# Optimization experiments

Hardware: AMD Instinct MI355X
Metric: run time of the kernel (lower is better)

Reference implementation:

```python
import jax, jax.numpy as jnp
import numpy as np
import math

SIZE = 64
NLAND = 8
N_ITER = 6


def setup_inputs() -> dict:
    key = jax.random.key(0)
    k1, k2, k3 = jax.random.split(key, 3)
    B, T, C = 4, 4096, 1024
    return {
        "q": jax.random.normal(k1, (B, T, C), dtype=jnp.float32),
        "k": jax.random.normal(k2, (B, T, C), dtype=jnp.float32),
        "v": jax.random.normal(k3, (B, T, C), dtype=jnp.float32),
    }


def _iterative_pinv(mat, n_iter=N_ITER):
    # Newton-Schulz iteration for pseudo-inverse of [..., m, m] kernel.
    m = mat.shape[-1]
    I = jnp.eye(m, dtype=mat.dtype)
    K = mat
    # NOTE: torch.max over the whole tensor (global scalar), faithful to source.
    V = (1.0 / jnp.max(jnp.sum(K, axis=-2))) * jnp.swapaxes(K, -1, -2)
    for _ in range(n_iter):
        KV = jnp.matmul(K, V)
        V = jnp.matmul(0.25 * V, 13.0 * I - jnp.matmul(KV, 15.0 * I - jnp.matmul(KV, 7.0 * I - KV)))
    return V


def reference(q, k, v):
    B, T, C = q.shape
    H = C // SIZE
    scale = 1.0 / math.sqrt(SIZE)
    # Faithful reshape (not transpose) as in the source module.
    qh = q.reshape(B, H, T, SIZE)
    kh = k.reshape(B, H, T, SIZE)
    vh = v.reshape(B, H, T, SIZE)
    # T % NLAND == 0 branch: landmark = segment mean over T//NLAND tokens.
    q_l = qh.reshape(B, H, NLAND, T // NLAND, SIZE).mean(axis=-2)  # [B,H,m,d]
    k_l = kh.reshape(B, H, NLAND, T // NLAND, SIZE).mean(axis=-2)
    kernel_1 = jax.nn.softmax(jnp.einsum('bhtd,bhmd->bhtm', qh, k_l) * scale, axis=-1)  # [B,H,T,m]
    kernel_2 = jax.nn.softmax(jnp.einsum('bhmd,bhnd->bhmn', q_l, k_l) * scale, axis=-1)  # [B,H,m,m]
    kernel_3 = jax.nn.softmax(jnp.einsum('bhmd,bhtd->bhmt', q_l, kh) * scale, axis=-1)  # [B,H,m,T]
    pinv = _iterative_pinv(kernel_2)  # [B,H,m,m]
    k3v = jnp.matmul(kernel_3, vh)    # [B,H,m,d]
    out = jnp.matmul(jnp.matmul(kernel_1, pinv), k3v)  # [B,H,T,d]
    return out.reshape(B, T, C)
```

## Files before the change

### kernel.cpp

```cpp
#include <hip/hip_runtime.h>
#include <math.h>

#define T_TOK 4096
#define DD 64
#define NHEADS 64
#define SEG 512
#define SCALE 0.125f

#define QL_OFF   0
#define KL_OFF   32768
#define K2_OFF   65536
#define CS_OFF   69632
#define PD_OFF   70144
#define W2_OFF   102912
#define KP_OFF   135680
#define PA_OFF   135680
#define P_OFF    659968

#define WAVE_BAR() __builtin_amdgcn_wave_barrier()

#define ROR_ADD(x, imm)                                                        \
  {                                                                            \
    int t_ = __builtin_amdgcn_update_dpp(0, __float_as_int(x), 0x120 | (imm),  \
                                         0xF, 0xF, false);                     \
    x += __int_as_float(t_);                                                   \
  }

__global__ __launch_bounds__(256) void qsum_kernel(
    const float* __restrict__ q, float* __restrict__ ws) {
  int tid = threadIdx.x;
  const float4* q4 = (const float4*)q + (size_t)blockIdx.x * 8192;
  float4 b[2][8];
#pragma unroll
  for (int i = 0; i < 8; ++i) b[0][i] = q4[i * 256 + tid];
  float4 a = make_float4(0.f, 0.f, 0.f, 0.f);
#pragma unroll
  for (int j = 0; j < 4; ++j) {
    if (j < 3) {
#pragma unroll
      for (int i = 0; i < 8; ++i)
        b[(j + 1) & 1][i] = q4[(j + 1) * 2048 + i * 256 + tid];
    }
#pragma unroll
    for (int i = 0; i < 8; ++i) {
      float4 x = b[j & 1][i];
      a.x += x.x; a.y += x.y; a.z += x.z; a.w += x.w;
    }
  }
  __shared__ float4 red[16][17];
  red[tid >> 4][tid & 15] = a;
  __syncthreads();
  if (tid < 16) {
    float4 s = make_float4(0.f, 0.f, 0.f, 0.f);
#pragma unroll
    for (int g = 0; g < 16; ++g) {
      float4 r = red[g][tid];
      s.x += r.x; s.y += r.y; s.z += r.z; s.w += r.w;
    }
    const float inv = 1.f / (float)SEG;
    s.x *= inv; s.y *= inv; s.z *= inv; s.w *= inv;
    ((float4*)(ws + QL_OFF))[blockIdx.x * 16 + tid] = s;
  }
}

__global__ __launch_bounds__(256, 4) void ppass_kernel(
    const float* __restrict__ k, float* __restrict__ ws) {
  int tid = threadIdx.x;
  int w = tid >> 6, lane = tid & 63;
  int gw = blockIdx.x * 4 + w;
  int hb = gw >> 6;
  int d16 = lane & 15, t4 = lane >> 4;

  float4 ql[8];
#pragma unroll
  for (int j = 0; j < 8; ++j)
    ql[j] = ((const float4*)(ws + QL_OFF))[hb * 128 + j * 16 + d16];

  size_t base4 = (size_t)gw * 1024;
  const float4* k4 = (const float4*)k + base4;
  float4* pP = (float4*)(ws + P_OFF) + (size_t)gw * 128;

  float den[8];
#pragma unroll
  for (int j = 0; j < 8; ++j) den[j] = 0.f;
  float4 ks = make_float4(0.f, 0.f, 0.f, 0.f);

#pragma unroll 2
  for (int it = 0; it < 16; ++it) {
    float4 kk = k4[it * 64 + lane];
    ks.x += kk.x; ks.y += kk.y; ks.z += kk.z; ks.w += kk.w;
    float dp[8];
#pragma unroll
    for (int j = 0; j < 8; ++j)
      dp[j] = kk.x * ql[j].x + kk.y * ql[j].y + kk.z * ql[j].z +
              kk.w * ql[j].w;
#pragma unroll
    for (int j = 0; j < 8; ++j) { ROR_ADD(dp[j], 8) }
#pragma unroll
    for (int j = 0; j < 8; ++j) { ROR_ADD(dp[j], 4) }
#pragma unroll
    for (int j = 0; j < 8; ++j) { ROR_ADD(dp[j], 2) }
#pragma unroll
    for (int j = 0; j < 8; ++j) { ROR_ADD(dp[j], 1) }
    float p[8];
#pragma unroll
    for (int j = 0; j < 8; ++j) {
      p[j] = __expf(dp[j] * SCALE);
      den[j] += p[j];
    }
    float4 lo = make_float4(p[0], p[1], p[2], p[3]);
    float4 hi = make_float4(p[4], p[5], p[6], p[7]);
    int tok2 = (it * 4 + t4) * 2;
    if (d16 == 0) pP[tok2] = lo;
    if (d16 == 1) pP[tok2 + 1] = hi;
  }

  ks.x += __shfl_xor(ks.x, 16, 64); ks.y += __shfl_xor(ks.y, 16, 64);
  ks.z += __shfl_xor(ks.z, 16, 64); ks.w += __shfl_xor(ks.w, 16, 64);
  ks.x += __shfl_xor(ks.x, 32, 64); ks.y += __shfl_xor(ks.y, 32, 64);
  ks.z += __shfl_xor(ks.z, 32, 64); ks.w += __shfl_xor(ks.w, 32, 64);
  if (lane < 16)
    ((float4*)(ws + KP_OFF))[gw * 16 + lane] = ks;
#pragma unroll
  for (int j = 0; j < 8; ++j) {
    den[j] += __shfl_xor(den[j], 16, 64);
    den[j] += __shfl_xor(den[j], 32, 64);
  }
  if (lane == 0) {
    *(float4*)&ws[PD_OFF + (size_t)gw * 8] =
        make_float4(den[0], den[1], den[2], den[3]);
    *(float4*)&ws[PD_OFF + (size_t)gw * 8 + 4] =
        make_float4(den[4], den[5], den[6], den[7]);
  }
}

__global__ __launch_bounds__(512) void prepk_kernel(float* __restrict__ ws) {
  int hb = blockIdx.x, tid = threadIdx.x;
  __shared__ float qls[8][68];
  __shared__ float kls[8][68];
  __shared__ float ee[8][9];
  int m = tid >> 6, d = tid & 63;
  float s = 0.f;
#pragma unroll
  for (int j = 0; j < 8; ++j)
    s += ws[KP_OFF + (size_t)(hb * 64 + m * 8 + j) * 64 + d];
  s *= (1.f / (float)SEG);
  kls[m][d] = s;
  ws[KL_OFF + hb * 512 + tid] = s;
  qls[m][d] = ws[QL_OFF + hb * 512 + tid];
  __syncthreads();
  if (tid < 64) {
    int i = tid >> 3, j = tid & 7;
    float dot = 0.f;
#pragma unroll
    for (int dd = 0; dd < 64; ++dd) dot += qls[i][dd] * kls[j][dd];
    ee[i][j] = __expf(dot * SCALE);
  }
  __syncthreads();
  if (tid < 64) {
    int i = tid >> 3, j = tid & 7;
    float ssum = 0.f;
#pragma unroll
    for (int jj = 0; jj < 8; ++jj) ssum += ee[i][jj];
    ws[K2_OFF + hb * 64 + tid] = ee[i][j] / ssum;
  }
  if (tid < 8) {
    float cs = 0.f;
    for (int ii = 0; ii < 8; ++ii) {
      float ssum = 0.f;
#pragma unroll
      for (int jj = 0; jj < 8; ++jj) ssum += ee[ii][jj];
      cs += ee[ii][tid] / ssum;
    }
    ws[CS_OFF + hb * 8 + tid] = cs;
  }
}

__global__ __launch_bounds__(256, 4) void vpass_kernel(
    const float* __restrict__ v, float* __restrict__ ws) {
  int tid = threadIdx.x;
  int w = tid >> 6, lane = tid & 63;
  int chunk = blockIdx.x;
  int gw = chunk * 4 + w;
  int t4 = lane >> 4;

  size_t base4 = (size_t)gw * 1024;
  const float4* v4 = (const float4*)v + base4;
  const float4* pP = (const float4*)(ws + P_OFF) + (size_t)gw * 128;

  float4 acc[8];
#pragma unroll
  for (int j = 0; j < 8; ++j) acc[j] = make_float4(0.f, 0.f, 0.f, 0.f);

#pragma unroll 2
  for (int it = 0; it < 16; ++it) {
    float4 vv = v4[it * 64 + lane];
    int tok2 = (it * 4 + t4) * 2;
    float4 plo = pP[tok2];
    float4 phi = pP[tok2 + 1];
    acc[0].x += plo.x*vv.x; acc[0].y += plo.x*vv.y; acc[0].z += plo.x*vv.z; acc[0].w += plo.x*vv.w;
    acc[1].x += plo.y*vv.x; acc[1].y += plo.y*vv.y; acc[1].z += plo.y*vv.z; acc[1].w += plo.y*vv.w;
    acc[2].x += plo.z*vv.x; acc[2].y += plo.z*vv.y; acc[2].z += plo.z*vv.z; acc[2].w += plo.z*vv.w;
    acc[3].x += plo.w*vv.x; acc[3].y += plo.w*vv.y; acc[3].z += plo.w*vv.z; acc[3].w += plo.w*vv.w;
    acc[4].x += phi.x*vv.x; acc[4].y += phi.x*vv.y; acc[4].z += phi.x*vv.z; acc[4].w += phi.x*vv.w;
    acc[5].x += phi.y*vv.x; acc[5].y += phi.y*vv.y; acc[5].z += phi.y*vv.z; acc[5].w += phi.y*vv.w;
    acc[6].x += phi.z*vv.x; acc[6].y += phi.z*vv.y; acc[6].z += phi.z*vv.z; acc[6].w += phi.z*vv.w;
    acc[7].x += phi.w*vv.x; acc[7].y += phi.w*vv.y; acc[7].z += phi.w*vv.z; acc[7].w += phi.w*vv.w;
  }

#pragma unroll
  for (int j = 0; j < 8; ++j) {
    acc[j].x += __shfl_xor(acc[j].x, 16, 64);
    acc[j].y += __shfl_xor(acc[j].y, 16, 64);
    acc[j].z += __shfl_xor(acc[j].z, 16, 64);
    acc[j].w += __shfl_xor(acc[j].w, 16, 64);
    acc[j].x += __shfl_xor(acc[j].x, 32, 64);
    acc[j].y += __shfl_xor(acc[j].y, 32, 64);
    acc[j].z += __shfl_xor(acc[j].z, 32, 64);
    acc[j].w += __shfl_xor(acc[j].w, 32, 64);
  }
  __shared__ float4 accred[4][8][17];
  if (lane < 16) {
#pragma unroll
    for (int j = 0; j < 8; ++j) accred[w][j][lane] = acc[j];
  }
  __syncthreads();
  if (tid < 128) {
    int m = tid >> 4, i = tid & 15;
    float4 a = accred[0][m][i], b = accred[1][m][i];
    float4 c = accred[2][m][i], d2 = accred[3][m][i];
    float4 s = make_float4(a.x + b.x + c.x + d2.x, a.y + b.y + c.y + d2.y,
                           a.z + b.z + c.z + d2.z, a.w + b.w + c.w + d2.w);
    ((float4*)(ws + PA_OFF))[((size_t)chunk * 8 + m) * 16 + i] = s;
  }
}

__global__ __launch_bounds__(512) void pinvw2_kernel(float* __restrict__ ws) {
  int hb = blockIdx.x, tid = threadIdx.x;
  __shared__ float k3vs[8][68];
  __shared__ float K[8][9], V[8][9], X[8][9], Y[8][9];
  __shared__ float smax;
  int m = tid >> 6, d = tid & 63;
  float s = 0.f, den = 0.f;
  for (int c = 0; c < 16; ++c)
    s += ws[PA_OFF + (((size_t)hb * 16 + c) * 8 + m) * 64 + d];
  for (int c = 0; c < 64; ++c)
    den += ws[PD_OFF + ((size_t)hb * 64 + c) * 8 + m];
  k3vs[m][d] = s / den;
  if (tid < 64) {
    float mx = 0.f;
    for (int t = 0; t < 8; ++t) mx = fmaxf(mx, ws[CS_OFF + t * 64 + tid]);
    for (int off = 32; off; off >>= 1) mx = fmaxf(mx, __shfl_xor(mx, off, 64));
    if (tid == 0) smax = mx;
  }
  int i = (tid >> 3) & 7, j = tid & 7;
  if (tid < 64) K[i][j] = ws[K2_OFF + hb * 64 + tid];
  __syncthreads();
  if (tid < 64) V[i][j] = K[j][i] * (1.f / smax);
  __syncthreads();
  for (int it = 0; it < 6; ++it) {
    float x = 0.f;
    if (tid < 64) {
      for (int kk = 0; kk < 8; ++kk) x += K[i][kk] * V[kk][j];
      X[i][j] = x;
    }
    __syncthreads();
    float bm = 0.f;
    if (tid < 64) {
      for (int kk = 0; kk < 8; ++kk) bm += X[i][kk] * X[kk][j];
      bm = 7.f * x - bm;
      Y[i][j] = bm;
    }
    __syncthreads();
    float dm = 0.f;
    if (tid < 64) {
      for (int kk = 0; kk < 8; ++kk) dm += X[i][kk] * Y[kk][j];
      dm = 15.f * x - dm;
    }
    __syncthreads();
    if (tid < 64) Y[i][j] = dm;
    __syncthreads();
    float vd = 0.f;
    if (tid < 64) {
      for (int kk = 0; kk < 8; ++kk) vd += V[i][kk] * Y[kk][j];
      vd = 0.25f * (13.f * V[i][j] - vd);
    }
    __syncthreads();
    if (tid < 64) V[i][j] = vd;
    __syncthreads();
  }
  float o = 0.f;
#pragma unroll
  for (int jj = 0; jj < 8; ++jj) o += V[m][jj] * k3vs[jj][d];
  ws[W2_OFF + hb * 512 + tid] = o;
}

__global__ __launch_bounds__(256) void out_kernel(
    const float* __restrict__ q, float* __restrict__ out,
    const float* __restrict__ ws) {
  int tid = threadIdx.x;
  int w = tid >> 6, lane = tid & 63;
  int gw = blockIdx.x * 4 + w;
  int hb = gw >> 6;
  __shared__ float qt_all[4][16][68];
  __shared__ float pl_all[4][16][9];
  __shared__ float w2_all[4][8][68];
  float (*qt)[68] = qt_all[w];
  float (*pl)[9]  = pl_all[w];
  float (*w2)[68] = w2_all[w];

  int m = lane & 7;
  float4 klrow[16];
#pragma unroll
  for (int d4 = 0; d4 < 16; ++d4)
    klrow[d4] = ((const float4*)(ws + KL_OFF))[hb * 128 + m * 16 + d4];
#pragma unroll
  for (int i = 0; i < 2; ++i) {
    int f4 = i * 64 + lane;
    float4 y = ((const float4*)(ws + W2_OFF))[hb * 128 + f4];
    *(float4*)&w2[f4 >> 4][(f4 & 15) * 4] = y;
  }

  size_t base4 = (size_t)gw * 1024;
  const float4* q4 = (const float4*)q + base4;
  float4* o4 = (float4*)out + base4;
  float4 buf[2][4];
#pragma unroll
  for (int i = 0; i < 4; ++i) buf[0][i] = q4[i * 64 + lane];

#pragma unroll
  for (int tile = 0; tile < 4; ++tile) {
    int cur = tile & 1;
    if (tile < 3) {
#pragma unroll
      for (int i = 0; i < 4; ++i)
        buf[cur ^ 1][i] = q4[(tile + 1) * 256 + i * 64 + lane];
    }
#pragma unroll
    for (int i = 0; i < 4; ++i) {
      int f4 = i * 64 + lane;
      *(float4*)&qt[f4 >> 4][(f4 & 15) * 4] = buf[cur][i];
    }
    WAVE_BAR();
#pragma unroll
    for (int rep = 0; rep < 2; ++rep) {
      int t = rep * 8 + (lane >> 3);
      const float4* qr = (const float4*)&qt[t][0];
      float dot = 0.f;
#pragma unroll
      for (int d4 = 0; d4 < 16; ++d4) {
        float4 a = qr[d4];
        dot += a.x * klrow[d4].x + a.y * klrow[d4].y +
               a.z * klrow[d4].z + a.w * klrow[d4].w;
      }
      pl[t][m] = __expf(dot * SCALE);
    }
    WAVE_BAR();
#pragma unroll
    for (int i = 0; i < 4; ++i) {
      int t = i * 4 + (lane >> 4);
      int qd = lane & 15;
      float p0 = pl[t][0], p1 = pl[t][1], p2 = pl[t][2], p3 = pl[t][3];
      float p4 = pl[t][4], p5 = pl[t][5], p6 = pl[t][6], p7 = pl[t][7];
      float inv = 1.f / (p0 + p1 + p2 + p3 + p4 + p5 + p6 + p7);
      float4 acc = make_float4(0.f, 0.f, 0.f, 0.f);
      float pm[8] = {p0, p1, p2, p3, p4, p5, p6, p7};
#pragma unroll
      for (int m2 = 0; m2 < 8; ++m2) {
        float wgt = pm[m2] * inv;
        float4 wv = *(const float4*)&w2[m2][qd * 4];
        acc.x += wgt * wv.x; acc.y += wgt * wv.y;
        acc.z += wgt * wv.z; acc.w += wgt * wv.w;
      }
      o4[tile * 256 + i * 64 + lane] = acc;
    }
    WAVE_BAR();
  }
}

extern "C" void kernel_launch(void* const* d_in, const int* in_sizes, int n_in,
                              void* d_out, int out_size, void* d_ws, size_t ws_size,
                              hipStream_t stream) {
  const float* q = (const float*)d_in[0];
  const float* k = (const float*)d_in[1];
  const float* v = (const float*)d_in[2];
  float* out = (float*)d_out;
  float* ws = (float*)d_ws;

  qsum_kernel<<<512, 256, 0, stream>>>(q, ws);
  ppass_kernel<<<1024, 256, 0, stream>>>(k, ws);
  prepk_kernel<<<NHEADS, 512, 0, stream>>>(ws);
  vpass_kernel<<<1024, 256, 0, stream>>>(v, ws);
  pinvw2_kernel<<<NHEADS, 512, 0, stream>>>(ws);
  out_kernel<<<1024, 256, 0, stream>>>(q, out, ws);
}
```

Before: 93.79 us.

## Fuse K softmax-weight pass and V accumulation into a single kvpass kernel

Merges the k pass, which computed kernel_3 exp weights and stored them to workspace, with the v pass, which reread those weights to accumulate kernel_3·V. Each wave now keeps the weights in registers and accumulates against V directly. This removes the intermediate P buffer round trip and one kernel launch. Per-wave partials are written out unreduced, and pinvw2 now reduces over 64 wave partials instead of 16 block partials. The trade-off is higher register pressure and more partial traffic in the final reduction.

```diff
diff --git a/kernel.cpp b/kernel.cpp
--- a/kernel.cpp
+++ b/kernel.cpp
@@ -11,11 +11,10 @@
 #define KL_OFF   32768
 #define K2_OFF   65536
 #define CS_OFF   69632
-#define PD_OFF   70144
-#define W2_OFF   102912
-#define KP_OFF   135680
-#define PA_OFF   135680
-#define P_OFF    659968
+#define KP_OFF   70144
+#define PA_OFF   332288
+#define PD_OFF   2429440
+#define W2_OFF   2462208
 
 #define WAVE_BAR() __builtin_amdgcn_wave_barrier()
 
@@ -63,13 +62,35 @@
   }
 }
 
-__global__ __launch_bounds__(256, 4) void ppass_kernel(
-    const float* __restrict__ k, float* __restrict__ ws) {
+#define KV_PROC(KK, VV)                                                        \
+  {                                                                            \
+    ks.x += KK.x; ks.y += KK.y; ks.z += KK.z; ks.w += KK.w;                    \
+    float dp[8];                                                               \
+    _Pragma("unroll")                                                          \
+    for (int j = 0; j < 8; ++j)                                                \
+      dp[j] = KK.x * ql[j].x + KK.y * ql[j].y + KK.z * ql[j].z +               \
+              KK.w * ql[j].w;                                                  \
+    _Pragma("unroll") for (int j = 0; j < 8; ++j) { ROR_ADD(dp[j], 8) }        \
+    _Pragma("unroll") for (int j = 0; j < 8; ++j) { ROR_ADD(dp[j], 4) }        \
+    _Pragma("unroll") for (int j = 0; j < 8; ++j) { ROR_ADD(dp[j], 2) }        \
+    _Pragma("unroll") for (int j = 0; j < 8; ++j) { ROR_ADD(dp[j], 1) }        \
+    _Pragma("unroll")                                                          \
+    for (int j = 0; j < 8; ++j) {                                              \
+      float p_ = __expf(dp[j] * SCALE);                                        \
+      den[j] += p_;                                                            \
+      acc[j].x += p_ * VV.x; acc[j].y += p_ * VV.y;                            \
+      acc[j].z += p_ * VV.z; acc[j].w += p_ * VV.w;                            \
+    }                                                                          \
+  }
+
+__global__ __launch_bounds__(256, 4) void kvpass_kernel(
+    const float* __restrict__ k, const float* __restrict__ v,
+    float* __restrict__ ws) {
   int tid = threadIdx.x;
   int w = tid >> 6, lane = tid & 63;
   int gw = blockIdx.x * 4 + w;
   int hb = gw >> 6;
-  int d16 = lane & 15, t4 = lane >> 4;
+  int d16 = lane & 15;
 
   float4 ql[8];
 #pragma unroll
@@ -78,134 +99,22 @@
 
   size_t base4 = (size_t)gw * 1024;
   const float4* k4 = (const float4*)k + base4;
-  float4* pP = (float4*)(ws + P_OFF) + (size_t)gw * 128;
-
+  const float4* v4 = (const float4*)v + base4;
+
+  float4 acc[8];
   float den[8];
 #pragma unroll
-  for (int j = 0; j < 8; ++j) den[j] = 0.f;
+  for (int j = 0; j < 8; ++j) {
+    acc[j] = make_float4(0.f, 0.f, 0.f, 0.f);
+    den[j] = 0.f;
+  }
   float4 ks = make_float4(0.f, 0.f, 0.f, 0.f);
 
 #pragma unroll 2
   for (int it = 0; it < 16; ++it) {
     float4 kk = k4[it * 64 + lane];
-    ks.x += kk.x; ks.y += kk.y; ks.z += kk.z; ks.w += kk.w;
-    float dp[8];
-#pragma unroll
-    for (int j = 0; j < 8; ++j)
-      dp[j] = kk.x * ql[j].x + kk.y * ql[j].y + kk.z * ql[j].z +
-              kk.w * ql[j].w;
-#pragma unroll
-    for (int j = 0; j < 8; ++j) { ROR_ADD(dp[j], 8) }
-#pragma unroll
-    for (int j = 0; j < 8; ++j) { ROR_ADD(dp[j], 4) }
-#pragma unroll
-    for (int j = 0; j < 8; ++j) { ROR_ADD(dp[j], 2) }
-#pragma unroll
-    for (int j = 0; j < 8; ++j) { ROR_ADD(dp[j], 1) }
-    float p[8];
-#pragma unroll
-    for (int j = 0; j < 8; ++j) {
-      p[j] = __expf(dp[j] * SCALE);
-      den[j] += p[j];
-    }
-    float4 lo = make_float4(p[0], p[1], p[2], p[3]);
-    float4 hi = make_float4(p[4], p[5], p[6], p[7]);
-    int tok2 = (it * 4 + t4) * 2;
-    if (d16 == 0) pP[tok2] = lo;
-    if (d16 == 1) pP[tok2 + 1] = hi;
-  }
-
-  ks.x += __shfl_xor(ks.x, 16, 64); ks.y += __shfl_xor(ks.y, 16, 64);
-  ks.z += __shfl_xor(ks.z, 16, 64); ks.w += __shfl_xor(ks.w, 16, 64);
-  ks.x += __shfl_xor(ks.x, 32, 64); ks.y += __shfl_xor(ks.y, 32, 64);
-  ks.z += __shfl_xor(ks.z, 32, 64); ks.w += __shfl_xor(ks.w, 32, 64);
-  if (lane < 16)
-    ((float4*)(ws + KP_OFF))[gw * 16 + lane] = ks;
-#pragma unroll
-  for (int j = 0; j < 8; ++j) {
-    den[j] += __shfl_xor(den[j], 16, 64);
-    den[j] += __shfl_xor(den[j], 32, 64);
-  }
-  if (lane == 0) {
-    *(float4*)&ws[PD_OFF + (size_t)gw * 8] =
-        make_float4(den[0], den[1], den[2], den[3]);
-    *(float4*)&ws[PD_OFF + (size_t)gw * 8 + 4] =
-        make_float4(den[4], den[5], den[6], den[7]);
-  }
-}
-
-__global__ __launch_bounds__(512) void prepk_kernel(float* __restrict__ ws) {
-  int hb = blockIdx.x, tid = threadIdx.x;
-  __shared__ float qls[8][68];
-  __shared__ float kls[8][68];
-  __shared__ float ee[8][9];
-  int m = tid >> 6, d = tid & 63;
-  float s = 0.f;
-#pragma unroll
-  for (int j = 0; j < 8; ++j)
-    s += ws[KP_OFF + (size_t)(hb * 64 + m * 8 + j) * 64 + d];
-  s *= (1.f / (float)SEG);
-  kls[m][d] = s;
-  ws[KL_OFF + hb * 512 + tid] = s;
-  qls[m][d] = ws[QL_OFF + hb * 512 + tid];
-  __syncthreads();
-  if (tid < 64) {
-    int i = tid >> 3, j = tid & 7;
-    float dot = 0.f;
-#pragma unroll
-    for (int dd = 0; dd < 64; ++dd) dot += qls[i][dd] * kls[j][dd];
-    ee[i][j] = __expf(dot * SCALE);
-  }
-  __syncthreads();
-  if (tid < 64) {
-    int i = tid >> 3, j = tid & 7;
-    float ssum = 0.f;
-#pragma unroll
-    for (int jj = 0; jj < 8; ++jj) ssum += ee[i][jj];
-    ws[K2_OFF + hb * 64 + tid] = ee[i][j] / ssum;
-  }
-  if (tid < 8) {
-    float cs = 0.f;
-    for (int ii = 0; ii < 8; ++ii) {
-      float ssum = 0.f;
-#pragma unroll
-      for (int jj = 0; jj < 8; ++jj) ssum += ee[ii][jj];
-      cs += ee[ii][tid] / ssum;
-    }
-    ws[CS_OFF + hb * 8 + tid] = cs;
-  }
-}
-
-__global__ __launch_bounds__(256, 4) void vpass_kernel(
-    const float* __restrict__ v, float* __restrict__ ws) {
-  int tid = threadIdx.x;
-  int w = tid >> 6, lane = tid & 63;
-  int chunk = blockIdx.x;
-  int gw = chunk * 4 + w;
-  int t4 = lane >> 4;
-
-  size_t base4 = (size_t)gw * 1024;
-  const float4* v4 = (const float4*)v + base4;
-  const float4* pP = (const float4*)(ws + P_OFF) + (size_t)gw * 128;
-
-  float4 acc[8];
-#pragma unroll
-  for (int j = 0; j < 8; ++j) acc[j] = make_float4(0.f, 0.f, 0.f, 0.f);
-
-#pragma unroll 2
-  for (int it = 0; it < 16; ++it) {
     float4 vv = v4[it * 64 + lane];
-    int tok2 = (it * 4 + t4) * 2;
-    float4 plo = pP[tok2];
-    float4 phi = pP[tok2 + 1];
-    acc[0].x += plo.x*vv.x; acc[0].y += plo.x*vv.y; acc[0].z += plo.x*vv.z; acc[0].w += plo.x*vv.w;
-    acc[1].x += plo.y*vv.x; acc[1].y += plo.y*vv.y; acc[1].z += plo.y*vv.z; acc[1].w += plo.y*vv.w;
-    acc[2].x += plo.z*vv.x; acc[2].y += plo.z*vv.y; acc[2].z += plo.z*vv.z; acc[2].w += plo.z*vv.w;
-    acc[3].x += plo.w*vv.x; acc[3].y += plo.w*vv.y; acc[3].z += plo.w*vv.z; acc[3].w += plo.w*vv.w;
-    acc[4].x += phi.x*vv.x; acc[4].y += phi.x*vv.y; acc[4].z += phi.x*vv.z; acc[4].w += phi.x*vv.w;
-    acc[5].x += phi.y*vv.x; acc[5].y += phi.y*vv.y; acc[5].z += phi.y*vv.z; acc[5].w += phi.y*vv.w;
-    acc[6].x += phi.z*vv.x; acc[6].y += phi.z*vv.y; acc[6].z += phi.z*vv.z; acc[6].w += phi.z*vv.w;
-    acc[7].x += phi.w*vv.x; acc[7].y += phi.w*vv.y; acc[7].z += phi.w*vv.z; acc[7].w += phi.w*vv.w;
+    KV_PROC(kk, vv)
   }
 
 #pragma unroll
@@ -218,20 +127,67 @@
     acc[j].y += __shfl_xor(acc[j].y, 32, 64);
     acc[j].z += __shfl_xor(acc[j].z, 32, 64);
     acc[j].w += __shfl_xor(acc[j].w, 32, 64);
-  }
-  __shared__ float4 accred[4][8][17];
+    den[j] += __shfl_xor(den[j], 16, 64);
+    den[j] += __shfl_xor(den[j], 32, 64);
+  }
+  ks.x += __shfl_xor(ks.x, 16, 64); ks.y += __shfl_xor(ks.y, 16, 64);
+  ks.z += __shfl_xor(ks.z, 16, 64); ks.w += __shfl_xor(ks.w, 16, 64);
+  ks.x += __shfl_xor(ks.x, 32, 64); ks.y += __shfl_xor(ks.y, 32, 64);
+  ks.z += __shfl_xor(ks.z, 32, 64); ks.w += __shfl_xor(ks.w, 32, 64);
+
   if (lane < 16) {
 #pragma unroll
-    for (int j = 0; j < 8; ++j) accred[w][j][lane] = acc[j];
-  }
-  __syncthreads();
-  if (tid < 128) {
-    int m = tid >> 4, i = tid & 15;
-    float4 a = accred[0][m][i], b = accred[1][m][i];
-    float4 c = accred[2][m][i], d2 = accred[3][m][i];
-    float4 s = make_float4(a.x + b.x + c.x + d2.x, a.y + b.y + c.y + d2.y,
-                           a.z + b.z + c.z + d2.z, a.w + b.w + c.w + d2.w);
-    ((float4*)(ws + PA_OFF))[((size_t)chunk * 8 + m) * 16 + i] = s;
+    for (int j = 0; j < 8; ++j)
+      ((float4*)(ws + PA_OFF))[((size_t)gw * 8 + j) * 16 + lane] = acc[j];
+    ((float4*)(ws + KP_OFF))[gw * 16 + lane] = ks;
+  }
+  if (lane == 0) {
+    *(float4*)&ws[PD_OFF + (size_t)gw * 8] =
+        make_float4(den[0], den[1], den[2], den[3]);
+    *(float4*)&ws[PD_OFF + (size_t)gw * 8 + 4] =
+        make_float4(den[4], den[5], den[6], den[7]);
+  }
+}
+
+__global__ __launch_bounds__(512) void prepk_kernel(float* __restrict__ ws) {
+  int hb = blockIdx.x, tid = threadIdx.x;
+  __shared__ float qls[8][68];
+  __shared__ float kls[8][68];
+  __shared__ float ee[8][9];
+  int m = tid >> 6, d = tid & 63;
+  float s = 0.f;
+#pragma unroll
+  for (int j = 0; j < 8; ++j)
+    s += ws[KP_OFF + (size_t)(hb * 64 + m * 8 + j) * 64 + d];
+  s *= (1.f / (float)SEG);
+  kls[m][d] = s;
+  ws[KL_OFF + hb * 512 + tid] = s;
+  qls[m][d] = ws[QL_OFF + hb * 512 + tid];
+  __syncthreads();
+  if (tid < 64) {
+    int i = tid >> 3, j = tid & 7;
+    float dot = 0.f;
+#pragma unroll
+    for (int dd = 0; dd < 64; ++dd) dot += qls[i][dd] * kls[j][dd];
+    ee[i][j] = __expf(dot * SCALE);
+  }
+  __syncthreads();
+  if (tid < 64) {
+    int i = tid >> 3, j = tid & 7;
+    float ssum = 0.f;
+#pragma unroll
+    for (int jj = 0; jj < 8; ++jj) ssum += ee[i][jj];
+    ws[K2_OFF + hb * 64 + tid] = ee[i][j] / ssum;
+  }
+  if (tid < 8) {
+    float cs = 0.f;
+    for (int ii = 0; ii < 8; ++ii) {
+      float ssum = 0.f;
+#pragma unroll
+      for (int jj = 0; jj < 8; ++jj) ssum += ee[ii][jj];
+      cs += ee[ii][tid] / ssum;
+    }
+    ws[CS_OFF + hb * 8 + tid] = cs;
   }
 }
 
@@ -242,10 +198,10 @@
   __shared__ float smax;
   int m = tid >> 6, d = tid & 63;
   float s = 0.f, den = 0.f;
-  for (int c = 0; c < 16; ++c)
-    s += ws[PA_OFF + (((size_t)hb * 16 + c) * 8 + m) * 64 + d];
-  for (int c = 0; c < 64; ++c)
+  for (int c = 0; c < 64; ++c) {
+    s += ws[PA_OFF + (((size_t)hb * 64 + c) * 8 + m) * 64 + d];
     den += ws[PD_OFF + ((size_t)hb * 64 + c) * 8 + m];
+  }
   k3vs[m][d] = s / den;
   if (tid < 64) {
     float mx = 0.f;
@@ -388,9 +344,8 @@
   float* ws = (float*)d_ws;
 
   qsum_kernel<<<512, 256, 0, stream>>>(q, ws);
-  ppass_kernel<<<1024, 256, 0, stream>>>(k, ws);
+  kvpass_kernel<<<1024, 256, 0, stream>>>(k, v, ws);
   prepk_kernel<<<NHEADS, 512, 0, stream>>>(ws);
-  vpass_kernel<<<1024, 256, 0, stream>>>(v, ws);
   pinvw2_kernel<<<NHEADS, 512, 0, stream>>>(ws);
   out_kernel<<<1024, 256, 0, stream>>>(q, out, ws);
 }
```

Measured after the change: 87.43 us. -6.8%, faster.
